# Performance work log

Hardware: AMD Instinct MI355X
Metric: run time of the kernel (lower is better)

## Reference

```python
import jax, jax.numpy as jnp
import numpy as np

N, IN_F, OUT_F, H = 4096, 128, 64, 8


def setup_inputs() -> dict:
    key = jax.random.key(0)
    k1, k2, k3, k4 = jax.random.split(key, 4)
    input_A = jax.random.normal(k1, (N, IN_F), jnp.float32)
    # linear_proj.weight: [H*OUT_F, IN_F] (torch Linear convention), xavier-ish scale
    Wp = jax.random.normal(k2, (H * OUT_F, IN_F), jnp.float32) * (1.0 / np.sqrt(IN_F))
    a_src = jax.random.normal(k3, (H, OUT_F), jnp.float32) * 0.1
    a_tgt = jax.random.normal(k4, (H, OUT_F), jnp.float32) * 0.1
    # dense additive mask (0 = connected); zeros => fully-connected graph, same math path
    adj_mask = jnp.zeros((N, N), jnp.float32)
    return {"input_A": input_A, "adj_mask": adj_mask, "Wp": Wp, "a_src": a_src, "a_tgt": a_tgt}


def reference(input_A, adj_mask, Wp, a_src, a_tgt):
    # dropout is identity in eval mode
    xp = (input_A @ Wp.T).reshape(-1, H, OUT_F)          # [N, H, F]
    ss = jnp.einsum('nhf,hf->hn', xp, a_src)             # scores_source, [H, N]
    st = jnp.einsum('nhf,hf->hn', xp, a_tgt)             # scores_target, [H, N]
    scores = jax.nn.leaky_relu(ss[:, :, None] + st[:, None, :], negative_slope=0.2)  # [H, N, N]
    attn = jax.nn.softmax(scores + adj_mask[None, :, :], axis=-1)                    # [H, N, N]
    out = jnp.einsum('hnm,mhf->nhf', attn, xp)           # bmm aggregate, [N, H, F]
    out = out.mean(axis=1)                               # mean over heads, [N, F]
    return jax.nn.relu(out)
```

## Files before the change

kernel.cpp:

```cpp
#include <hip/hip_runtime.h>
#include <hip/hip_bf16.h>
#include <cstdint>

#define GN 4096
#define GIN 128
#define GF 64
#define GH 8
#define GHF (GH*GF)
#define LOG2E 1.4426950408889634f

typedef __attribute__((ext_vector_type(8))) short short8v;
typedef __attribute__((ext_vector_type(4))) float f32x4;

__device__ __forceinline__ short f2bf(float x) {
    uint32_t u = __float_as_uint(x);
    uint32_t r = u + 0x7fffu + ((u >> 16) & 1u);
    return (short)(r >> 16);
}
__device__ __forceinline__ uint32_t pack_bf16_rh(float lo, float hi) {
    uint32_t a = __float_as_uint(lo) + 0x8000u;
    uint32_t b = __float_as_uint(hi) + 0x8000u;
    return __builtin_amdgcn_perm(b, a, 0x07060302u);
}
__device__ __forceinline__ float leaky(float t) { return fmaxf(t, 0.2f * t); }

__global__ void gat_zeroflag(uint32_t* __restrict__ f) {
    if (threadIdx.x == 0 && blockIdx.x == 0) f[0] = 0u;
}

__global__ __launch_bounds__(256) void gat_proj(const float* __restrict__ A,
                                                const float* __restrict__ W,
                                                const float* __restrict__ a_src,
                                                const float* __restrict__ a_tgt,
                                                const uint32_t* __restrict__ maskbits,
                                                float* __restrict__ ss,
                                                float* __restrict__ st,
                                                short* __restrict__ bh,
                                                uint32_t* __restrict__ mflag) {
    __shared__ float lds[2 * 64 * 129];
    float* As = lds;
    float* Ws = lds + 64 * 129;
    const int n0 = blockIdx.x * 64;
    const int h  = blockIdx.y;
    const int j0 = h * 64;
    const int tid = threadIdx.x;
    const float4* A4 = (const float4*)A;
    const float4* W4 = (const float4*)W;
#pragma unroll
    for (int i = 0; i < 8; ++i) {
        int idx = tid + i * 256;
        int r = idx >> 5, c4 = idx & 31;
        float4 v = A4[(size_t)(n0 + r) * 32 + c4];
        As[r * 129 + c4 * 4 + 0] = v.x; As[r * 129 + c4 * 4 + 1] = v.y;
        As[r * 129 + c4 * 4 + 2] = v.z; As[r * 129 + c4 * 4 + 3] = v.w;
        float4 w = W4[(size_t)(j0 + r) * 32 + c4];
        Ws[r * 129 + c4 * 4 + 0] = w.x; Ws[r * 129 + c4 * 4 + 1] = w.y;
        Ws[r * 129 + c4 * 4 + 2] = w.z; Ws[r * 129 + c4 * 4 + 3] = w.w;
    }
    __syncthreads();
    const int tx = tid & 15, ty = tid >> 4;
    float acc[4][4] = {};
    for (int k = 0; k < 128; ++k) {
        float a[4], b[4];
#pragma unroll
        for (int i = 0; i < 4; ++i) { a[i] = As[(ty * 4 + i) * 129 + k]; b[i] = Ws[(tx * 4 + i) * 129 + k]; }
#pragma unroll
        for (int i = 0; i < 4; ++i)
#pragma unroll
            for (int j = 0; j < 4; ++j) acc[i][j] = fmaf(a[i], b[j], acc[i][j]);
    }
    __syncthreads();
    float* X = lds;
#pragma unroll
    for (int i = 0; i < 4; ++i)
#pragma unroll
        for (int j = 0; j < 4; ++j)
            X[(ty * 4 + i) * 65 + tx * 4 + j] = acc[i][j];
    __syncthreads();

    const int lane = tid & 63, w = tid >> 6;
    float s1 = 0.f, s2 = 0.f;
#pragma unroll
    for (int k = 0; k < 16; ++k) {
        int f = w * 16 + k;
        float x = X[lane * 65 + f];
        s1 = fmaf(x, a_src[j0 + f], s1);
        s2 = fmaf(x, a_tgt[j0 + f], s2);
    }
    float* ps = lds + 64 * 129;
    ps[w * 64 + lane] = s1;
    ps[(4 + w) * 64 + lane] = s2;
    __syncthreads();
    if (w == 0) {
        ss[h * GN + n0 + lane] = ps[lane] + ps[64 + lane] + ps[128 + lane] + ps[192 + lane];
        st[h * GN + n0 + lane] = ps[256 + lane] + ps[320 + lane] + ps[384 + lane] + ps[448 + lane];
    }

#pragma unroll
    for (int rep = 0; rep < 2; ++rep) {
        int fid = tid + rep * 256;
        int t_local = fid >> 8, cf = (fid >> 6) & 3, lf = fid & 63;
        int gg = lf >> 4, c = lf & 15;
        short8v vh;
#pragma unroll
        for (int jj = 0; jj < 8; ++jj)
            vh[jj] = f2bf(X[(t_local * 32 + gg * 8 + jj) * 65 + cf * 16 + c]);
        ((short8v*)bh)[((size_t)(h * 128 + (n0 >> 5) + t_local) * 4 + cf) * 64 + lf] = vh;
    }

    uint32_t accOr = 0;
    const uint4* m4 = (const uint4*)maskbits;
    const int nblocks = gridDim.x * gridDim.y;
    const int bid = blockIdx.y * gridDim.x + blockIdx.x;
    const int total = (GN * GN) / 4;
    for (int i = bid * 256 + tid; i < total; i += nblocks * 256) {
        uint4 v = m4[i];
        accOr |= v.x | v.y | v.z | v.w;
    }
#pragma unroll
    for (int d = 1; d < 64; d <<= 1) accOr |= (uint32_t)__shfl_xor((int)accOr, d);
    if ((tid & 63) == 0 && accOr) atomicOr(mflag, 1u);
}

__global__ __launch_bounds__(256) void gat_stmax(const float* __restrict__ st,
                                                 float* __restrict__ stmax) {
    const int h = blockIdx.x;
    const int tid = threadIdx.x;
    float m = -1e30f;
    for (int i = tid; i < GN; i += 256) m = fmaxf(m, st[h * GN + i]);
#pragma unroll
    for (int d = 1; d < 64; d <<= 1) m = fmaxf(m, __shfl_xor(m, d));
    __shared__ float wred[4];
    if ((tid & 63) == 0) wred[tid >> 6] = m;
    __syncthreads();
    if (tid == 0)
        stmax[h] = fmaxf(fmaxf(wred[0], wred[1]), fmaxf(wred[2], wred[3]));
}

__global__ __launch_bounds__(256) void gat_attn_fast(const short* __restrict__ bh,
                                                     const float* __restrict__ ss,
                                                     const float* __restrict__ st,
                                                     const float* __restrict__ stmax,
                                                     const uint32_t* __restrict__ mflag,
                                                     float* __restrict__ acc_p,
                                                     float* __restrict__ l_p,
                                                     int S) {
    if (mflag[0] != 0u) return;
    const int lane = threadIdx.x & 63;
    const int h = blockIdx.y * 4 + (threadIdx.x >> 6);
    const int q0 = blockIdx.x * 64;
    const int s = blockIdx.z;
    const int TPS = 128 / S;
    const int g = lane >> 4;
    const int c = lane & 15;

    const float smx = stmax[h];
    float EP[4], EN[4];
#pragma unroll
    for (int qf = 0; qf < 4; ++qf) {
        float ssa = ss[h * GN + q0 + qf * 16 + c];
        float caL = leaky(ssa + smx) * LOG2E;
        EP[qf] = __builtin_amdgcn_exp2f(fmaf(ssa, LOG2E, -caL));
        EN[qf] = __builtin_amdgcn_exp2f(fmaf(0.2f * ssa, LOG2E, -caL));
    }

    const short BONE = (short)0x3F80;
    const short8v BONES = {BONE, BONE, BONE, BONE, BONE, BONE, BONE, BONE};

    f32x4 acc[4][4];
    f32x4 accL[4];
#pragma unroll
    for (int qf = 0; qf < 4; ++qf) {
        accL[qf] = (f32x4){0.f, 0.f, 0.f, 0.f};
#pragma unroll
        for (int cf = 0; cf < 4; ++cf) acc[qf][cf] = (f32x4){0.f, 0.f, 0.f, 0.f};
    }

    const int t0 = s * TPS;
    const float4* stp = (const float4*)&st[h * GN + t0 * 32 + g * 8];
    const short8v* bhp = (const short8v*)bh + ((size_t)(h * 128 + t0) * 4) * 64 + lane;

    float4 sA[2]; short8v HA[4];
    float4 sB[2]; short8v HB[4];

#define LOADT(sv, Hv) do {                                      \
    sv[0] = stp[0]; sv[1] = stp[1]; stp += 8;                   \
    _Pragma("unroll")                                           \
    for (int i = 0; i < 4; ++i) Hv[i] = bhp[i * 64];            \
    bhp += 256; } while (0)

#define COMPUTET(sv, Hv) do {                                               \
    float stvL[8] = {sv[0].x * LOG2E, sv[0].y * LOG2E, sv[0].z * LOG2E,     \
                     sv[0].w * LOG2E, sv[1].x * LOG2E, sv[1].y * LOG2E,     \
                     sv[1].z * LOG2E, sv[1].w * LOG2E};                     \
    float e1[8], e2[8];                                                     \
    _Pragma("unroll")                                                       \
    for (int j = 0; j < 8; ++j) {                                           \
        e1[j] = __builtin_amdgcn_exp2f(stvL[j]);                            \
        e2[j] = __builtin_amdgcn_exp2f(0.2f * stvL[j]);                     \
    }                                                                       \
    _Pragma("unroll")                                                       \
    for (int qf = 0; qf < 4; ++qf) {                                        \
        float pa[8];                                                        \
        _Pragma("unroll")                                                   \
        for (int j = 0; j < 8; ++j)                                         \
            pa[j] = fmaxf(e1[j] * EP[qf], e2[j] * EN[qf]);                  \
        union { uint32_t u[4]; short8v v; } P;                              \
        _Pragma("unroll")                                                   \
        for (int w2 = 0; w2 < 4; ++w2)                                      \
            P.u[w2] = pack_bf16_rh(pa[2 * w2], pa[2 * w2 + 1]);             \
        _Pragma("unroll")                                                   \
        for (int cf = 0; cf < 4; ++cf)                                      \
            acc[qf][cf] = __builtin_amdgcn_mfma_f32_16x16x32_bf16(P.v, Hv[cf], acc[qf][cf], 0, 0, 0); \
        accL[qf] = __builtin_amdgcn_mfma_f32_16x16x32_bf16(P.v, BONES, accL[qf], 0, 0, 0); \
    } } while (0)

    LOADT(sA, HA);
    for (int t = 0; t + 2 < TPS; t += 2) {
        LOADT(sB, HB);
        COMPUTET(sA, HA);
        LOADT(sA, HA);
        COMPUTET(sB, HB);
    }
    LOADT(sB, HB);
    COMPUTET(sA, HA);
    COMPUTET(sB, HB);

#undef LOADT
#undef COMPUTET

    if (c == 0) {
#pragma unroll
        for (int qf = 0; qf < 4; ++qf)
#pragma unroll
            for (int r = 0; r < 4; ++r)
                l_p[(size_t)(s * GH + h) * GN + q0 + qf * 16 + g * 4 + r] = accL[qf][r];
    }
#pragma unroll
    for (int qf = 0; qf < 4; ++qf)
#pragma unroll
        for (int cf = 0; cf < 4; ++cf)
#pragma unroll
            for (int r = 0; r < 4; ++r)
                acc_p[((size_t)(s * GH + h) * GN + q0 + qf * 16 + g * 4 + r) * GF + cf * 16 + c]
                    = acc[qf][cf][r];
}

__global__ __launch_bounds__(256) void gat_attn_mask(const short* __restrict__ bh,
                                                     const float* __restrict__ ss,
                                                     const float* __restrict__ st,
                                                     const float* __restrict__ stmax,
                                                     const float* __restrict__ mask,
                                                     const uint32_t* __restrict__ mflag,
                                                     float* __restrict__ acc_p,
                                                     float* __restrict__ l_p,
                                                     int S) {
    if (mflag[0] == 0u) return;
    const int lane = threadIdx.x & 63;
    const int h = blockIdx.y * 4 + (threadIdx.x >> 6);
    const int q0 = blockIdx.x * 16;
    const int s = blockIdx.z;
    const int TPS = 128 / S;
    const int g = lane >> 4;

    const int qa = q0 + (lane & 15);
    const float ssa = ss[h * GN + qa];
    const float smx = stmax[h];
    const float caL = leaky(ssa + smx) * LOG2E;
    const float KaP = fmaf(ssa, LOG2E, -caL), KaN = fmaf(0.2f * ssa, LOG2E, -caL);

    const short BONE = (short)0x3F80;
    const short8v BONES = {BONE, BONE, BONE, BONE, BONE, BONE, BONE, BONE};

    f32x4 acc[4];
#pragma unroll
    for (int cf = 0; cf < 4; ++cf) acc[cf] = (f32x4){0.f, 0.f, 0.f, 0.f};
    f32x4 accL = (f32x4){0.f, 0.f, 0.f, 0.f};

    const int t0 = s * TPS;
    const float4* stp = (const float4*)&st[h * GN + t0 * 32 + g * 8];
    const float4* mpa = (const float4*)&mask[(size_t)qa * GN + t0 * 32 + g * 8];
    const short8v* bhp = (const short8v*)bh + ((size_t)(h * 128 + t0) * 4) * 64 + lane;

    for (int t = 0; t < TPS; ++t) {
        float4 s0 = stp[0], s1 = stp[1]; stp += 8;
        float4 a0 = mpa[0], a1 = mpa[1]; mpa += 8;
        short8v H[4];
#pragma unroll
        for (int i = 0; i < 4; ++i) H[i] = bhp[i * 64];
        bhp += 256;
        float stv[8] = {s0.x, s0.y, s0.z, s0.w, s1.x, s1.y, s1.z, s1.w};
        float mav[8] = {a0.x, a0.y, a0.z, a0.w, a1.x, a1.y, a1.z, a1.w};
        float pa[8];
#pragma unroll
        for (int j = 0; j < 8; ++j) {
            float stvL = stv[j] * LOG2E;
            float ea = fmaxf(stvL + KaP, fmaf(stvL, 0.2f, KaN));
            ea = fmaf(mav[j], LOG2E, ea);
            pa[j] = __builtin_amdgcn_exp2f(ea);
        }
        union { uint32_t u[4]; short8v v; } P;
#pragma unroll
        for (int w2 = 0; w2 < 4; ++w2) P.u[w2] = pack_bf16_rh(pa[2 * w2], pa[2 * w2 + 1]);
#pragma unroll
        for (int cf = 0; cf < 4; ++cf)
            acc[cf] = __builtin_amdgcn_mfma_f32_16x16x32_bf16(P.v, H[cf], acc[cf], 0, 0, 0);
        accL = __builtin_amdgcn_mfma_f32_16x16x32_bf16(P.v, BONES, accL, 0, 0, 0);
    }

    if ((lane & 15) == 0) {
#pragma unroll
        for (int r = 0; r < 4; ++r)
            l_p[(size_t)(s * GH + h) * GN + q0 + g * 4 + r] = accL[r];
    }
#pragma unroll
    for (int cf = 0; cf < 4; ++cf)
#pragma unroll
        for (int r = 0; r < 4; ++r)
            acc_p[((size_t)(s * GH + h) * GN + q0 + g * 4 + r) * GF + cf * 16 + (lane & 15)]
                = acc[cf][r];
}

__global__ __launch_bounds__(256) void gat_combine(const float* __restrict__ acc_p,
                                                   const float* __restrict__ l_p,
                                                   float* __restrict__ out, int S) {
    const int idx = blockIdx.x * 256 + threadIdx.x;
    const int n = idx >> 4, f4 = idx & 15;
    const float4* ap = (const float4*)acc_p;
    float4 r = {0.f, 0.f, 0.f, 0.f};
#pragma unroll
    for (int h = 0; h < GH; ++h) {
        float4 a = {0.f, 0.f, 0.f, 0.f};
        float l = 0.f;
        for (int s = 0; s < S; ++s) {
            float4 v = ap[((size_t)(s * GH + h) * GN + n) * 16 + f4];
            a.x += v.x; a.y += v.y; a.z += v.z; a.w += v.w;
            l += l_p[(size_t)(s * GH + h) * GN + n];
        }
        float il = 1.0f / l;
        r.x += a.x * il; r.y += a.y * il; r.z += a.z * il; r.w += a.w * il;
    }
    float4 o;
    o.x = fmaxf(r.x * 0.125f, 0.f);
    o.y = fmaxf(r.y * 0.125f, 0.f);
    o.z = fmaxf(r.z * 0.125f, 0.f);
    o.w = fmaxf(r.w * 0.125f, 0.f);
    ((float4*)out)[idx] = o;
}

extern "C" void kernel_launch(void* const* d_in, const int* in_sizes, int n_in,
                              void* d_out, int out_size, void* d_ws, size_t ws_size,
                              hipStream_t stream) {
    const float* A     = (const float*)d_in[0];
    const float* mask  = (const float*)d_in[1];
    const float* Wp    = (const float*)d_in[2];
    const float* a_src = (const float*)d_in[3];
    const float* a_tgt = (const float*)d_in[4];
    float* out = (float*)d_out;

    char* w = (char*)d_ws;
    float* ss    = (float*)w;              w += (size_t)GH * GN * 4;
    float* st    = (float*)w;              w += (size_t)GH * GN * 4;
    float* stmx  = (float*)w;              w += 256;
    uint32_t* mflag = (uint32_t*)w;        w += 256;
    short* bh    = (short*)w;              w += (size_t)GH * 128 * 4 * 64 * 8 * 2;
    size_t base = (size_t)(w - (char*)d_ws);
    size_t per_s = (size_t)GH * GN * GF * 4 + (size_t)GH * GN * 4;
    int S = 4;
    while (S > 1 && base + (size_t)S * per_s > ws_size) S >>= 1;
    float* acc_p = (float*)w;              w += (size_t)S * GH * GN * GF * 4;
    float* l_p   = (float*)w;

    gat_zeroflag<<<1, 64, 0, stream>>>(mflag);
    gat_proj<<<dim3(GN / 64, GH), 256, 0, stream>>>(A, Wp, a_src, a_tgt,
                                                    (const uint32_t*)mask,
                                                    ss, st, bh, mflag);
    gat_stmax<<<GH, 256, 0, stream>>>(st, stmx);
    gat_attn_fast<<<dim3(GN / 64, 2, S), 256, 0, stream>>>(bh, ss, st, stmx,
                                                           mflag, acc_p, l_p, S);
    gat_attn_mask<<<dim3(GN / 16, 2, S), 256, 0, stream>>>(bh, ss, st, stmx, mask,
                                                           mflag, acc_p, l_p, S);
    gat_combine<<<(GN * 16) / 256, 256, 0, stream>>>(acc_p, l_p, out, S);
}
```

Measured before the change: 83.86 us.

## Precompute key exponentials in projection and fuse stmax via atomicMax

The projection kernel now writes exp2 of the target scores and of 0.2 times them, so the attention inner loop no longer evaluates exponentials per key. The per-head max of target scores is computed with a wave reduction and an atomicMax on sign-flipped float encodings, which removes the separate stmax kernel launch. The trade is extra global reads of two float arrays instead of one in the attention loop, plus a few atomics in the projection kernel.

```diff
diff --git a/kernel.cpp b/kernel.cpp
--- a/kernel.cpp
+++ b/kernel.cpp
@@ -23,9 +23,18 @@
     return __builtin_amdgcn_perm(b, a, 0x07060302u);
 }
 __device__ __forceinline__ float leaky(float t) { return fmaxf(t, 0.2f * t); }
-
-__global__ void gat_zeroflag(uint32_t* __restrict__ f) {
-    if (threadIdx.x == 0 && blockIdx.x == 0) f[0] = 0u;
+__device__ __forceinline__ uint32_t fenc(float f) {
+    uint32_t u = __float_as_uint(f);
+    return (u & 0x80000000u) ? ~u : (u | 0x80000000u);
+}
+__device__ __forceinline__ float fdec(uint32_t k) {
+    uint32_t u = (k & 0x80000000u) ? (k ^ 0x80000000u) : ~k;
+    return __uint_as_float(u);
+}
+
+__global__ void gat_zeroflag(uint32_t* __restrict__ f, uint32_t* __restrict__ stmaxi) {
+    if (blockIdx.x == 0 && threadIdx.x == 0) f[0] = 0u;
+    if (blockIdx.x == 0 && threadIdx.x < GH) stmaxi[threadIdx.x] = 0u;
 }
 
 __global__ __launch_bounds__(256) void gat_proj(const float* __restrict__ A,
@@ -35,6 +44,9 @@
                                                 const uint32_t* __restrict__ maskbits,
                                                 float* __restrict__ ss,
                                                 float* __restrict__ st,
+                                                float* __restrict__ e1,
+                                                float* __restrict__ e2,
+                                                uint32_t* __restrict__ stmaxi,
                                                 short* __restrict__ bh,
                                                 uint32_t* __restrict__ mflag) {
     __shared__ float lds[2 * 64 * 129];
@@ -92,8 +104,17 @@
     ps[(4 + w) * 64 + lane] = s2;
     __syncthreads();
     if (w == 0) {
-        ss[h * GN + n0 + lane] = ps[lane] + ps[64 + lane] + ps[128 + lane] + ps[192 + lane];
-        st[h * GN + n0 + lane] = ps[256 + lane] + ps[320 + lane] + ps[384 + lane] + ps[448 + lane];
+        float ssv = ps[lane] + ps[64 + lane] + ps[128 + lane] + ps[192 + lane];
+        float stv = ps[256 + lane] + ps[320 + lane] + ps[384 + lane] + ps[448 + lane];
+        ss[h * GN + n0 + lane] = ssv;
+        st[h * GN + n0 + lane] = stv;
+        float stL = stv * LOG2E;
+        e1[h * GN + n0 + lane] = __builtin_amdgcn_exp2f(stL);
+        e2[h * GN + n0 + lane] = __builtin_amdgcn_exp2f(0.2f * stL);
+        float m = stv;
+#pragma unroll
+        for (int d = 1; d < 64; d <<= 1) m = fmaxf(m, __shfl_xor(m, d));
+        if (lane == 0) atomicMax(&stmaxi[h], fenc(m));
     }
 
 #pragma unroll
@@ -122,25 +143,11 @@
     if ((tid & 63) == 0 && accOr) atomicOr(mflag, 1u);
 }
 
-__global__ __launch_bounds__(256) void gat_stmax(const float* __restrict__ st,
-                                                 float* __restrict__ stmax) {
-    const int h = blockIdx.x;
-    const int tid = threadIdx.x;
-    float m = -1e30f;
-    for (int i = tid; i < GN; i += 256) m = fmaxf(m, st[h * GN + i]);
-#pragma unroll
-    for (int d = 1; d < 64; d <<= 1) m = fmaxf(m, __shfl_xor(m, d));
-    __shared__ float wred[4];
-    if ((tid & 63) == 0) wred[tid >> 6] = m;
-    __syncthreads();
-    if (tid == 0)
-        stmax[h] = fmaxf(fmaxf(wred[0], wred[1]), fmaxf(wred[2], wred[3]));
-}
-
 __global__ __launch_bounds__(256) void gat_attn_fast(const short* __restrict__ bh,
                                                      const float* __restrict__ ss,
-                                                     const float* __restrict__ st,
-                                                     const float* __restrict__ stmax,
+                                                     const float* __restrict__ e1,
+                                                     const float* __restrict__ e2,
+                                                     const uint32_t* __restrict__ stmaxi,
                                                      const uint32_t* __restrict__ mflag,
                                                      float* __restrict__ acc_p,
                                                      float* __restrict__ l_p,
@@ -154,7 +161,7 @@
     const int g = lane >> 4;
     const int c = lane & 15;
 
-    const float smx = stmax[h];
+    const float smx = fdec(stmaxi[h]);
     float EP[4], EN[4];
 #pragma unroll
     for (int qf = 0; qf < 4; ++qf) {
@@ -177,34 +184,31 @@
     }
 
     const int t0 = s * TPS;
-    const float4* stp = (const float4*)&st[h * GN + t0 * 32 + g * 8];
+    const float4* e1p = (const float4*)&e1[h * GN + t0 * 32 + g * 8];
+    const float4* e2p = (const float4*)&e2[h * GN + t0 * 32 + g * 8];
     const short8v* bhp = (const short8v*)bh + ((size_t)(h * 128 + t0) * 4) * 64 + lane;
 
-    float4 sA[2]; short8v HA[4];
-    float4 sB[2]; short8v HB[4];
-
-#define LOADT(sv, Hv) do {                                      \
-    sv[0] = stp[0]; sv[1] = stp[1]; stp += 8;                   \
+    float4 eA[2], fA[2]; short8v HA[4];
+    float4 eB[2], fB[2]; short8v HB[4];
+
+#define LOADT(Ev, Fv, Hv) do {                                  \
+    Ev[0] = e1p[0]; Ev[1] = e1p[1]; e1p += 8;                   \
+    Fv[0] = e2p[0]; Fv[1] = e2p[1]; e2p += 8;                   \
     _Pragma("unroll")                                           \
     for (int i = 0; i < 4; ++i) Hv[i] = bhp[i * 64];            \
     bhp += 256; } while (0)
 
-#define COMPUTET(sv, Hv) do {                                               \
-    float stvL[8] = {sv[0].x * LOG2E, sv[0].y * LOG2E, sv[0].z * LOG2E,     \
-                     sv[0].w * LOG2E, sv[1].x * LOG2E, sv[1].y * LOG2E,     \
-                     sv[1].z * LOG2E, sv[1].w * LOG2E};                     \
-    float e1[8], e2[8];                                                     \
-    _Pragma("unroll")                                                       \
-    for (int j = 0; j < 8; ++j) {                                           \
-        e1[j] = __builtin_amdgcn_exp2f(stvL[j]);                            \
-        e2[j] = __builtin_amdgcn_exp2f(0.2f * stvL[j]);                     \
-    }                                                                       \
+#define COMPUTET(Ev, Fv, Hv) do {                                           \
+    float e1v[8] = {Ev[0].x, Ev[0].y, Ev[0].z, Ev[0].w,                     \
+                    Ev[1].x, Ev[1].y, Ev[1].z, Ev[1].w};                    \
+    float e2v[8] = {Fv[0].x, Fv[0].y, Fv[0].z, Fv[0].w,                     \
+                    Fv[1].x, Fv[1].y, Fv[1].z, Fv[1].w};                    \
     _Pragma("unroll")                                                       \
     for (int qf = 0; qf < 4; ++qf) {                                        \
         float pa[8];                                                        \
         _Pragma("unroll")                                                   \
         for (int j = 0; j < 8; ++j)                                         \
-            pa[j] = fmaxf(e1[j] * EP[qf], e2[j] * EN[qf]);                  \
+            pa[j] = fmaxf(e1v[j] * EP[qf], e2v[j] * EN[qf]);                \
         union { uint32_t u[4]; short8v v; } P;                              \
         _Pragma("unroll")                                                   \
         for (int w2 = 0; w2 < 4; ++w2)                                      \
@@ -215,16 +219,16 @@
         accL[qf] = __builtin_amdgcn_mfma_f32_16x16x32_bf16(P.v, BONES, accL[qf], 0, 0, 0); \
     } } while (0)
 
-    LOADT(sA, HA);
+    LOADT(eA, fA, HA);
     for (int t = 0; t + 2 < TPS; t += 2) {
-        LOADT(sB, HB);
-        COMPUTET(sA, HA);
-        LOADT(sA, HA);
-        COMPUTET(sB, HB);
-    }
-    LOADT(sB, HB);
-    COMPUTET(sA, HA);
-    COMPUTET(sB, HB);
+        LOADT(eB, fB, HB);
+        COMPUTET(eA, fA, HA);
+        LOADT(eA, fA, HA);
+        COMPUTET(eB, fB, HB);
+    }
+    LOADT(eB, fB, HB);
+    COMPUTET(eA, fA, HA);
+    COMPUTET(eB, fB, HB);
 
 #undef LOADT
 #undef COMPUTET
@@ -249,7 +253,7 @@
 __global__ __launch_bounds__(256) void gat_attn_mask(const short* __restrict__ bh,
                                                      const float* __restrict__ ss,
                                                      const float* __restrict__ st,
-                                                     const float* __restrict__ stmax,
+                                                     const uint32_t* __restrict__ stmaxi,
                                                      const float* __restrict__ mask,
                                                      const uint32_t* __restrict__ mflag,
                                                      float* __restrict__ acc_p,
@@ -265,7 +269,7 @@
 
     const int qa = q0 + (lane & 15);
     const float ssa = ss[h * GN + qa];
-    const float smx = stmax[h];
+    const float smx = fdec(stmaxi[h]);
     const float caL = leaky(ssa + smx) * LOG2E;
     const float KaP = fmaf(ssa, LOG2E, -caL), KaN = fmaf(0.2f * ssa, LOG2E, -caL);
 
@@ -361,8 +365,10 @@
     char* w = (char*)d_ws;
     float* ss    = (float*)w;              w += (size_t)GH * GN * 4;
     float* st    = (float*)w;              w += (size_t)GH * GN * 4;
-    float* stmx  = (float*)w;              w += 256;
-    uint32_t* mflag = (uint32_t*)w;        w += 256;
+    float* e1    = (float*)w;              w += (size_t)GH * GN * 4;
+    float* e2    = (float*)w;              w += (size_t)GH * GN * 4;
+    uint32_t* stmaxi = (uint32_t*)w;       w += 256;
+    uint32_t* mflag  = (uint32_t*)w;       w += 256;
     short* bh    = (short*)w;              w += (size_t)GH * 128 * 4 * 64 * 8 * 2;
     size_t base = (size_t)(w - (char*)d_ws);
     size_t per_s = (size_t)GH * GN * GF * 4 + (size_t)GH * GN * 4;
@@ -371,14 +377,13 @@
     float* acc_p = (float*)w;              w += (size_t)S * GH * GN * GF * 4;
     float* l_p   = (float*)w;
 
-    gat_zeroflag<<<1, 64, 0, stream>>>(mflag);
+    gat_zeroflag<<<1, 64, 0, stream>>>(mflag, stmaxi);
     gat_proj<<<dim3(GN / 64, GH), 256, 0, stream>>>(A, Wp, a_src, a_tgt,
                                                     (const uint32_t*)mask,
-                                                    ss, st, bh, mflag);
-    gat_stmax<<<GH, 256, 0, stream>>>(st, stmx);
-    gat_attn_fast<<<dim3(GN / 64, 2, S), 256, 0, stream>>>(bh, ss, st, stmx,
+                                                    ss, st, e1, e2, stmaxi, bh, mflag);
+    gat_attn_fast<<<dim3(GN / 64, 2, S), 256, 0, stream>>>(bh, ss, e1, e2, stmaxi,
                                                            mflag, acc_p, l_p, S);
-    gat_attn_mask<<<dim3(GN / 16, 2, S), 256, 0, stream>>>(bh, ss, st, stmx, mask,
+    gat_attn_mask<<<dim3(GN / 16, 2, S), 256, 0, stream>>>(bh, ss, st, stmaxi, mask,
                                                            mflag, acc_p, l_p, S);
     gat_combine<<<(GN * 16) / 256, 256, 0, stream>>>(acc_p, l_p, out, S);
 }
```

Result: slower. 101.8 us (+21.4%).
